# Kernel optimization log

Hardware: AMD Instinct MI355X
Metric: run time of the kernel (lower is better)

Reference implementation:

```python
import jax, jax.numpy as jnp
import numpy as np
from jax import lax

B = 65536
T = 512
DT = 0.05


def setup_inputs() -> dict:
    key = jax.random.key(0)
    k1, k2 = jax.random.split(key)
    y0 = jax.random.uniform(k1, (B, 2), dtype=jnp.float32)  # positive biomass/substrate
    t_eval = jnp.arange(T, dtype=jnp.float32) * DT
    D_seq = jax.random.uniform(k2, (T - 1,), dtype=jnp.float32)
    K_m = jnp.float32(0.12)
    s_e = jnp.float32(10.0)
    mu_max = jnp.float32(0.4)
    return {"y0": y0, "t_eval": t_eval, "D_seq": D_seq,
            "K_m": K_m, "s_e": s_e, "mu_max": mu_max}


def reference(y0, t_eval, D_seq, K_m, s_e, mu_max):
    # RK4 integration of the Monod chemostat ODE, y: (..., 2) = (b, s)
    def rhs(y, D):
        b, s = y[..., 0], y[..., 1]
        rho = mu_max * s / (K_m + s)
        dbdt = -D * b + rho * b
        dsdt = D * (s_e - s) - rho * b
        return jnp.stack([dbdt, dsdt], axis=-1)

    dts = t_eval[1:] - t_eval[:-1]          # (T-1,)
    D = D_seq[: t_eval.shape[0] - 1]         # use D_seq[i] for step i

    def step(y, inp):
        dt, D_i = inp
        k1 = rhs(y, D_i)
        k2 = rhs(y + dt / 2 * k1, D_i)
        k3 = rhs(y + dt / 2 * k2, D_i)
        k4 = rhs(y + dt * k3, D_i)
        y_next = y + dt / 6 * (k1 + 2 * k2 + 2 * k3 + k4)
        return y_next, y_next

    _, ys = lax.scan(step, y0, (dts, D))     # ys: (T-1, B, 2)
    return jnp.concatenate([y0[None], ys], axis=0)  # (T, B, 2)
```

## Files before the change

kernel.cpp:

```cpp
#include <hip/hip_runtime.h>

#define NB 65536
#define NT 512

typedef float f32x2 __attribute__((ext_vector_type(2)));

__global__ __launch_bounds__(256) void rk4_biosystem_kernel(
    const float* __restrict__ y0,
    const float* __restrict__ t_eval,
    const float* __restrict__ D_seq,
    const float* __restrict__ K_m_p,
    const float* __restrict__ s_e_p,
    const float* __restrict__ mu_max_p,
    float* __restrict__ out)
{
    __shared__ float s_dt[NT - 1];
    __shared__ float s_D[NT - 1];

    const int tid = threadIdx.x;
    for (int i = tid; i < NT - 1; i += 256) {
        s_dt[i] = t_eval[i + 1] - t_eval[i];
        s_D[i]  = D_seq[i];
    }
    __syncthreads();

    const float K_m    = K_m_p[0];
    const float s_e    = s_e_p[0];
    const float mu_max = mu_max_p[0];

    const int traj = blockIdx.x * 256 + tid;

    float b = y0[traj * 2 + 0];
    float s = y0[traj * 2 + 1];

    f32x2* __restrict__ out2 = (f32x2*)out;

    {
        f32x2 v; v.x = b; v.y = s;
        out2[traj] = v;
    }

    float dt0 = s_dt[0], D0 = s_D[0];
    float dt1 = s_dt[1], D1 = s_D[1];

    #define RHS(bb, ss, db, ds)                                  \
        {                                                        \
            float inv = __builtin_amdgcn_rcpf(K_m + (ss));       \
            float num = (mu_max * (ss)) * (bb);                  \
            float rb  = num * inv;                               \
            db = __builtin_fmaf(-D, (bb), rb);                   \
            ds = __builtin_fmaf(D, s_e - (ss), -rb);             \
        }

    #pragma unroll 8
    for (int t = 0; t < NT - 1; ++t) {
        const float dt = dt0;
        const float D  = D0;
        dt0 = dt1; D0 = D1;
        const int tn = (t < NT - 3) ? (t + 2) : (NT - 2);
        dt1 = s_dt[tn];
        D1  = s_D[tn];

        float k1b, k1s, k2b, k2s, k3b, k3s, k4b, k4s;
        RHS(b, s, k1b, k1s);
        const float h2 = dt * 0.5f;
        RHS(__builtin_fmaf(h2, k1b, b), __builtin_fmaf(h2, k1s, s), k2b, k2s);
        RHS(__builtin_fmaf(h2, k2b, b), __builtin_fmaf(h2, k2s, s), k3b, k3s);
        RHS(__builtin_fmaf(dt, k3b, b), __builtin_fmaf(dt, k3s, s), k4b, k4s);

        const float sb  = (k1b + k4b) + 2.0f * (k2b + k3b);
        const float ss_ = (k1s + k4s) + 2.0f * (k2s + k3s);
        const float h6 = dt * (1.0f / 6.0f);
        b = __builtin_fmaf(h6, sb, b);
        s = __builtin_fmaf(h6, ss_, s);

        f32x2 v; v.x = b; v.y = s;
        out2[(t + 1) * NB + traj] = v;
    }
    #undef RHS
}

extern "C" void kernel_launch(void* const* d_in, const int* in_sizes, int n_in,
                              void* d_out, int out_size, void* d_ws, size_t ws_size,
                              hipStream_t stream) {
    const float* y0     = (const float*)d_in[0];
    const float* t_eval = (const float*)d_in[1];
    const float* D_seq  = (const float*)d_in[2];
    const float* K_m    = (const float*)d_in[3];
    const float* s_e    = (const float*)d_in[4];
    const float* mu_max = (const float*)d_in[5];
    float* out = (float*)d_out;

    dim3 grid(NB / 256);
    dim3 block(256);
    rk4_biosystem_kernel<<<grid, block, 0, stream>>>(y0, t_eval, D_seq, K_m, s_e, mu_max, out);
}
```

Measured before the change: 63.31 us.

## Use half-wave active lanes and packed f32x2 FMAs in RK4 loop

Each 64-wide wavefront now keeps only its first 32 lanes active, with twice as many blocks launched so every trajectory is still covered. The RK4 arithmetic is rewritten with two-wide vector FMAs on the (b, s) pair so the compiler can emit packed FP32 instructions. The apparent aim is to change how wave slots, issue and store coalescing are balanced in this store-bound kernel. The cost is that half the lanes sit idle and twice as many blocks each reload the shared dt/D tables.

```diff
diff --git a/kernel.cpp b/kernel.cpp
--- a/kernel.cpp
+++ b/kernel.cpp
@@ -2,8 +2,13 @@
 
 #define NB 65536
 #define NT 512
+#define TPB 128
 
 typedef float f32x2 __attribute__((ext_vector_type(2)));
+
+static __device__ __forceinline__ f32x2 fma2(f32x2 a, f32x2 b, f32x2 c) {
+    return __builtin_elementwise_fma(a, b, c);
+}
 
 __global__ __launch_bounds__(256) void rk4_biosystem_kernel(
     const float* __restrict__ y0,
@@ -24,33 +29,23 @@
     }
     __syncthreads();
 
+    if ((tid & 63) >= 32) return;
+
     const float K_m    = K_m_p[0];
     const float s_e    = s_e_p[0];
     const float mu_max = mu_max_p[0];
 
-    const int traj = blockIdx.x * 256 + tid;
+    const int traj = blockIdx.x * TPB + (tid >> 6) * 32 + (tid & 31);
 
-    float b = y0[traj * 2 + 0];
-    float s = y0[traj * 2 + 1];
+    const f32x2* __restrict__ y0v = (const f32x2*)y0;
+    f32x2 y = y0v[traj];
 
     f32x2* __restrict__ out2 = (f32x2*)out;
-
-    {
-        f32x2 v; v.x = b; v.y = s;
-        out2[traj] = v;
-    }
+    out2[traj] = y;
+    f32x2* __restrict__ op = out2 + traj;
 
     float dt0 = s_dt[0], D0 = s_D[0];
     float dt1 = s_dt[1], D1 = s_D[1];
-
-    #define RHS(bb, ss, db, ds)                                  \
-        {                                                        \
-            float inv = __builtin_amdgcn_rcpf(K_m + (ss));       \
-            float num = (mu_max * (ss)) * (bb);                  \
-            float rb  = num * inv;                               \
-            db = __builtin_fmaf(-D, (bb), rb);                   \
-            ds = __builtin_fmaf(D, s_e - (ss), -rb);             \
-        }
 
     #pragma unroll 8
     for (int t = 0; t < NT - 1; ++t) {
@@ -61,23 +56,38 @@
         dt1 = s_dt[tn];
         D1  = s_D[tn];
 
-        float k1b, k1s, k2b, k2s, k3b, k3s, k4b, k4s;
-        RHS(b, s, k1b, k1s);
+        auto rhs = [&](f32x2 yi) -> f32x2 {
+            const float bi = yi.x, si = yi.y;
+            const float inv = __builtin_amdgcn_rcpf(K_m + si);
+            const float num = (mu_max * si) * bi;
+            const float rb  = num * inv;
+            f32x2 coef; coef.x = -D;  coef.y = D;
+            f32x2 vec;  vec.x  = bi;  vec.y  = s_e - si;
+            f32x2 addn; addn.x = rb;  addn.y = -rb;
+            return fma2(coef, vec, addn);
+        };
+
         const float h2 = dt * 0.5f;
-        RHS(__builtin_fmaf(h2, k1b, b), __builtin_fmaf(h2, k1s, s), k2b, k2s);
-        RHS(__builtin_fmaf(h2, k2b, b), __builtin_fmaf(h2, k2s, s), k3b, k3s);
-        RHS(__builtin_fmaf(dt, k3b, b), __builtin_fmaf(dt, k3s, s), k4b, k4s);
+        f32x2 h2v; h2v.x = h2; h2v.y = h2;
+        f32x2 dtv; dtv.x = dt; dtv.y = dt;
 
-        const float sb  = (k1b + k4b) + 2.0f * (k2b + k3b);
-        const float ss_ = (k1s + k4s) + 2.0f * (k2s + k3s);
+        const f32x2 k1 = rhs(y);
+        const f32x2 k2 = rhs(fma2(h2v, k1, y));
+        const f32x2 k3 = rhs(fma2(h2v, k2, y));
+        const f32x2 k4 = rhs(fma2(dtv, k3, y));
+
+        const f32x2 t14 = k1 + k4;
+        const f32x2 t23 = k2 + k3;
+        f32x2 twov; twov.x = 2.0f; twov.y = 2.0f;
+        const f32x2 ksum = fma2(twov, t23, t14);
+
         const float h6 = dt * (1.0f / 6.0f);
-        b = __builtin_fmaf(h6, sb, b);
-        s = __builtin_fmaf(h6, ss_, s);
+        f32x2 h6v; h6v.x = h6; h6v.y = h6;
+        y = fma2(h6v, ksum, y);
 
-        f32x2 v; v.x = b; v.y = s;
-        out2[(t + 1) * NB + traj] = v;
+        op += NB;
+        *op = y;
     }
-    #undef RHS
 }
 
 extern "C" void kernel_launch(void* const* d_in, const int* in_sizes, int n_in,
@@ -91,7 +101,7 @@
     const float* mu_max = (const float*)d_in[5];
     float* out = (float*)d_out;
 
-    dim3 grid(NB / 256);
+    dim3 grid(NB / TPB);
     dim3 block(256);
     rk4_biosystem_kernel<<<grid, block, 0, stream>>>(y0, t_eval, D_seq, K_m, s_e, mu_max, out);
 }
```

Result: slower. 94.53 us (+49.3%).
